# Kernel tuning notes

Measured on AMD Instinct MI355X. Metric: run time of the kernel, lower is better.

Reference implementation:

```python
import jax, jax.numpy as jnp
import numpy as np

_MASK = -1.0e9
_EPS = 1e-8
B, N, E, D, L, NREL, TAU = 4, 2048, 32768, 128, 3, 1000, 0.1


def setup_inputs() -> dict:
    key = jax.random.key(0)
    ks = jax.random.split(key, 24)
    s = 0.05
    inp = {
        'edge_index': jax.random.randint(ks[0], (B, 2, E), 0, N, dtype=jnp.int32),
        'rels': jax.random.randint(ks[1], (B, E), 0, NREL, dtype=jnp.int32),
        'scores': jax.random.uniform(ks[2], (B, E), dtype=jnp.float32),
        'edge_conf_mask': jax.random.randint(ks[3], (B, E), 0, 2) > 0,
        'edge_mask': jax.random.randint(ks[4], (B, E), 0, 2) > 0,
        'mask': jnp.ones((B, N), dtype=bool),
        'r_query_embed': jax.random.normal(ks[5], (B, D), dtype=jnp.float32),
        'conf_embeds': jax.random.normal(ks[6], (B, E, D), dtype=jnp.float32),
        'rel_table': jax.random.normal(ks[7], (NREL, D), dtype=jnp.float32) * s,
        'beta_W': jax.random.normal(ks[8], (D, 1), dtype=jnp.float32) * s,
        'beta_b': jnp.zeros((1,), dtype=jnp.float32),
        'msg_W': jax.random.normal(ks[9], (L, 5 * D, D), dtype=jnp.float32) * s,
        'msg_b': jnp.zeros((L, D), dtype=jnp.float32),
        'upd_W': jax.random.normal(ks[10], (L, D, D), dtype=jnp.float32) * s,
        'upd_b': jnp.zeros((L, D), dtype=jnp.float32),
        'ln_g': jnp.ones((D,), dtype=jnp.float32),
        'ln_b': jnp.zeros((D,), dtype=jnp.float32),
        'att_W': jax.random.normal(ks[11], (L, 3 * D, 1), dtype=jnp.float32) * s,
        'att_b': jnp.zeros((L, 1), dtype=jnp.float32),
        'den_W1': jax.random.normal(ks[12], (3 * D, D), dtype=jnp.float32) * s,
        'den_b1': jnp.zeros((D,), dtype=jnp.float32),
        'den_W2': jax.random.normal(ks[13], (D, 1), dtype=jnp.float32) * s,
        'den_b2': jnp.zeros((1,), dtype=jnp.float32),
    }
    return inp


def _layer_norm(x, g, b, eps=1e-5):
    mu = jnp.mean(x, axis=-1, keepdims=True)
    var = jnp.var(x, axis=-1, keepdims=True)
    return (x - mu) * jax.lax.rsqrt(var + eps) * g + b


def reference(edge_index, rels, scores, edge_conf_mask, edge_mask, mask,
              r_query_embed, conf_embeds, rel_table, beta_W, beta_b,
              msg_W, msg_b, upd_W, upd_b, ln_g, ln_b, att_W, att_b,
              den_W1, den_b1, den_W2, den_b2):
    Bb, Nn = mask.shape
    Ee = edge_index.shape[2]
    d = rel_table.shape[1]
    bidx = jnp.arange(Bb)[:, None]                      # [B,1] batch index for scatter/gather
    src = edge_index[:, 0, :]                           # [B,E]
    tgt = edge_index[:, 1, :]                           # [B,E]

    h_init = jnp.zeros((Bb, Nn, d), dtype=rel_table.dtype).at[:, 0, :].set(1.0)
    h = h_init
    h_r = rel_table[rels]                               # [B,E,D]
    rq = jnp.broadcast_to(r_query_embed[:, None, :], (Bb, Ee, d))
    em = edge_mask.astype(h.dtype)[..., None]           # [B,E,1]

    # edge denoiser gate
    gate_in = jnp.concatenate([h_r, rq, conf_embeds], axis=-1)
    den = jax.nn.sigmoid(jax.nn.relu(gate_in @ den_W1 + den_b1) @ den_W2 + den_b2) * em

    beta = jax.nn.sigmoid((h_r + rq) @ beta_W + beta_b)             # [B,E,1]
    gate_known = jax.nn.sigmoid((scores[..., None] - beta) / TAU)
    gate = jnp.where(edge_conf_mask[..., None], gate_known, 0.5)

    outs = []
    for k in range(msg_W.shape[0]):
        h_src = h[bidx, src]                            # [B,E,D] gather
        h_init_src = h_init[bidx, src]
        msg_in = jnp.concatenate([h_src * h_r, h_src, h_init_src, h_r, conf_embeds], axis=-1)
        raw_msg = jax.nn.relu(msg_in @ msg_W[k] + msg_b[k])         # [B,E,D]

        att_in = jnp.concatenate([raw_msg, h_r, rq], axis=-1)
        att = jax.nn.leaky_relu((att_in @ att_W[k] + att_b[k])[..., 0], 0.01)
        att = jnp.where(edge_mask, att, _MASK)

        # scatter-softmax over edges sharing a target node
        mx = jnp.full((Bb, Nn), _MASK, dtype=att.dtype).at[bidx, tgt].max(att)
        ex = jnp.exp(att - mx[bidx, tgt])
        sm = jnp.zeros((Bb, Nn), dtype=att.dtype).at[bidx, tgt].add(ex)
        alpha = ex / (sm[bidx, tgt] + _EPS)             # [B,E]

        wmsg = gate * alpha[..., None] * raw_msg * em * den
        aggr = jnp.zeros_like(h).at[bidx, tgt].add(wmsg)
        h = _layer_norm(h + aggr @ upd_W[k] + upd_b[k], ln_g, ln_b)
        outs.append(h[:, 0, :])
    return jnp.stack(outs, axis=1)                      # [B,L,D]
```

## Files before the change

kernel.cpp:

```cpp
#include <hip/hip_runtime.h>
#include <stdint.h>
#include <math.h>

#define BB 4
#define NNODE 2048
#define NE 32768
#define DDIM 128
#define NL 3
#define NRELS 1000
#define MASKV -1000000000.0f

typedef unsigned short ushort_t;
typedef __attribute__((ext_vector_type(8))) short bfrag;
typedef __attribute__((ext_vector_type(4))) float f4;

__device__ __forceinline__ float sigf(float x){ return 1.0f/(1.0f+expf(-x)); }

__device__ __forceinline__ float bf2f(ushort_t u){
  union { unsigned int i; float f; } v; v.i = ((unsigned int)u) << 16; return v.f;
}
__device__ __forceinline__ ushort_t f2bf(float x){
  union { float f; unsigned int u; } v; v.f = x;
  unsigned int r = (v.u + 0x7FFFu + ((v.u >> 16) & 1u)) >> 16;
  return (ushort_t)r;
}
__device__ __forceinline__ float bflo(unsigned u){
  union{unsigned i;float f;}v; v.i=u<<16; return v.f;
}
__device__ __forceinline__ float bfhi(unsigned u){
  union{unsigned i;float f;}v; v.i=u&0xFFFF0000u; return v.f;
}
__device__ __forceinline__ unsigned pmul_bf(unsigned a, unsigned b){
  return (unsigned)f2bf(bflo(a)*bflo(b)) | ((unsigned)f2bf(bfhi(a)*bfhi(b))<<16);
}
__device__ __forceinline__ unsigned packbf(float a, float b){
  return (unsigned)f2bf(a) | ((unsigned)f2bf(b)<<16);
}

__global__ void prep_kernel(const void* cm_raw, const void* em_raw,
    uint8_t* __restrict__ cm, uint8_t* __restrict__ em, int* __restrict__ deg,
    const float* __restrict__ relt, ushort_t* __restrict__ relt_bf,
    const float* __restrict__ rq, ushort_t* __restrict__ rq_bf,
    int* __restrict__ src_c, int* __restrict__ rel_c, int* __restrict__ ge_c,
    float* __restrict__ h, ushort_t* __restrict__ h_bf)
{
  __shared__ int flag_s;
  if (threadIdx.x < 64){
    unsigned v = ((const unsigned*)cm_raw)[threadIdx.x];
    bool i32ok = (v <= 1u);
    bool f32ok = (v == 0u) || (v == 0x3F800000u);
    unsigned long long bi = __ballot(i32ok);
    unsigned long long bf_ = __ballot(f32ok);
    if (threadIdx.x == 0) flag_s = (bi==~0ULL) ? 0 : ((bf_==~0ULL) ? 1 : 2);
  }
  __syncthreads();
  const int f = flag_s;
  int gid = blockIdx.x*256 + threadIdx.x;
  if (gid < BB*NE){
    uint8_t c, e;
    if (f == 0){ c = ((const int*)cm_raw)[gid]!=0;   e = ((const int*)em_raw)[gid]!=0; }
    else if (f == 1){ c = ((const float*)cm_raw)[gid]!=0.0f; e = ((const float*)em_raw)[gid]!=0.0f; }
    else { c = ((const uint8_t*)cm_raw)[gid]!=0; e = ((const uint8_t*)em_raw)[gid]!=0; }
    cm[gid]=c; em[gid]=e;
    src_c[gid]=0; rel_c[gid]=0; ge_c[gid]=0;
  }
  if (gid < BB*NNODE) deg[gid]=0;
  if (gid < NRELS*DDIM/4){
    float4 v = *(const float4*)&relt[gid*4];
    ushort4 o; o.x=f2bf(v.x); o.y=f2bf(v.y); o.z=f2bf(v.z); o.w=f2bf(v.w);
    *(ushort4*)&relt_bf[gid*4] = o;
  }
  if (gid < BB*DDIM/4){
    float4 v = *(const float4*)&rq[gid*4];
    ushort4 o; o.x=f2bf(v.x); o.y=f2bf(v.y); o.z=f2bf(v.z); o.w=f2bf(v.w);
    *(ushort4*)&rq_bf[gid*4] = o;
  }
  {
    int base = gid*4;
    int nd = base & (NNODE*DDIM - 1);
    bool one = (nd < DDIM);
    float4 hv = one ? (float4){1.f,1.f,1.f,1.f} : (float4){0.f,0.f,0.f,0.f};
    ushort4 hb = one ? (ushort4){0x3F80,0x3F80,0x3F80,0x3F80} : (ushort4){0,0,0,0};
    *(float4*)&h[base] = hv;
    *(ushort4*)&h_bf[base] = hb;
  }
}

__global__ void csr_hist_kernel(const int* __restrict__ edge_index,
                                const uint8_t* __restrict__ em, int* __restrict__ deg){
  int gid = blockIdx.x*256 + threadIdx.x;
  if (!em[gid]) return;
  int b = gid >> 15, e = gid & (NE-1);
  int tgt = edge_index[(b<<16) + NE + e];
  atomicAdd(&deg[(b<<11) + tgt], 1);
}
__global__ void csr_scan_kernel(const int* __restrict__ deg,
                                int* __restrict__ base, int* __restrict__ cursor){
  __shared__ int part[256];
  int t = threadIdx.x;
  int loc[32]; int s = 0;
  #pragma unroll
  for (int i=0;i<32;++i){ loc[i] = deg[t*32+i]; s += loc[i]; }
  part[t] = s; __syncthreads();
  for (int off=1; off<256; off<<=1){
    int v = (t >= off) ? part[t-off] : 0;
    __syncthreads();
    part[t] += v;
    __syncthreads();
  }
  int ex = (t==0) ? 0 : part[t-1];
  #pragma unroll
  for (int i=0;i<32;++i){ base[t*32+i] = ex; cursor[t*32+i] = ex; ex += loc[i]; }
  if (t == 255) base[256*32] = ex;
}
__global__ void csr_scatter_kernel(const int* __restrict__ edge_index,
                                   const int* __restrict__ rels,
                                   const uint8_t* __restrict__ em,
                                   int* __restrict__ cursor,
                                   int* __restrict__ src_c, int* __restrict__ rel_c,
                                   int* __restrict__ ge_c){
  int gid = blockIdx.x*256 + threadIdx.x;
  if (!em[gid]) return;
  int b = gid >> 15, e = gid & (NE-1);
  int tgt = edge_index[(b<<16) + NE + e];
  int src = edge_index[(b<<16) + e];
  int pos = atomicAdd(&cursor[(b<<11) + tgt], 1);
  src_c[pos] = (b<<11) | src;
  rel_c[pos] = rels[gid];
  ge_c[pos]  = gid;
}

__global__ void precomp_tables_kernel(
    const float* __restrict__ relt, const float* __restrict__ rq,
    const float* __restrict__ attW, const float* __restrict__ betaW,
    const float* __restrict__ msgW, const float* __restrict__ denW1,
    const float* __restrict__ denb1,
    float* __restrict__ att_rel, float* __restrict__ att_rq,
    float* __restrict__ beta_rel, float* __restrict__ beta_rq,
    float* __restrict__ denrq, float* __restrict__ initvec,
    float* __restrict__ src0vec)
{
  int wid = (blockIdx.x*256 + threadIdx.x) >> 6;
  int lane = threadIdx.x & 63;
  if (wid >= 4024) return;
  if (wid >= 4016){
    int widx = wid - 4016;
    const float* A = nullptr; const float* W; int K = 128;
    float* outp; const float* bias = nullptr;
    if (widx < 4){ A = rq + widx*128; W = denW1 + 16384; outp = denrq + widx*128; bias = denb1; }
    else if (widx < 7){ int k=widx-4; W = msgW + (size_t)k*81920 + 32768; outp = initvec + k*128; }
    else { W = msgW + 16384; K = 256; outp = src0vec; }
    float a0=0.f, a1=0.f;
    for (int kk=0; kk<K; kk+=8){
      float av[8], w0[8], w1[8];
      #pragma unroll
      for (int u=0;u<8;++u){
        av[u] = A ? A[kk+u] : 1.0f;
        w0[u] = W[(size_t)(kk+u)*128 + lane];
        w1[u] = W[(size_t)(kk+u)*128 + lane + 64];
      }
      #pragma unroll
      for (int u=0;u<8;++u){ a0 = fmaf(av[u], w0[u], a0); a1 = fmaf(av[u], w1[u], a1); }
    }
    if (bias){ a0 += bias[lane]; a1 += bias[lane+64]; }
    outp[lane] = a0; outp[lane+64] = a1;
    return;
  }
  const float* vec; const float* w; float* dst; int di;
  if (wid < 3*NRELS){
    int k = wid/1000, rl = wid%1000;
    vec = relt + rl*DDIM; w = attW + k*384 + 128; dst = att_rel; di = wid;
  } else if (wid < 3*NRELS + 3*BB){
    int idx = wid - 3*NRELS; int k = idx/BB, b = idx%BB;
    vec = rq + b*DDIM; w = attW + k*384 + 256; dst = att_rq; di = idx;
  } else if (wid < 3*NRELS + 3*BB + NRELS){
    int rl = wid - (3*NRELS + 3*BB);
    vec = relt + rl*DDIM; w = betaW; dst = beta_rel; di = rl;
  } else {
    int b = wid - (3*NRELS + 3*BB + NRELS);
    vec = rq + b*DDIM; w = betaW; dst = beta_rq; di = b;
  }
  float s = vec[lane]*w[lane] + vec[lane+64]*w[lane+64];
  #pragma unroll
  for (int off=32; off; off>>=1) s += __shfl_xor(s, off, 64);
  if (lane == 0) dst[di] = s;
}

__global__ void build_wimg_kernel(const float* __restrict__ msgW,
                                  const float* __restrict__ denW1,
                                  ushort_t* __restrict__ img_msg,
                                  ushort_t* __restrict__ img_den,
                                  ushort_t* __restrict__ img_tab){
  int e = blockIdx.x*256 + threadIdx.x;
  if (e >= 22*8192) return;
  int img_id = e >> 13;
  int ei = e & 8191;
  int j = ei >> 6;
  int kk = (((ei & 63) << 1) ^ ((j & 7) << 4)) >> 1;
  float v;
  ushort_t* dst;
  if (img_id < 12){
    int k = img_id >> 2, c = img_id & 3;
    int rowbase = (c < 2) ? c*64 : 512 + (c-2)*64;
    v = msgW[(size_t)k*81920 + (rowbase+kk)*128 + j];
    dst = img_msg + (size_t)img_id*8192;
  } else if (img_id < 14){
    int c = img_id - 12;
    v = denW1[(size_t)(256 + c*64 + kk)*128 + j];
    dst = img_den + (size_t)c*8192;
  } else if (img_id < 20){
    int idx = img_id - 14, k = idx >> 1, c = idx & 1;
    v = msgW[(size_t)k*81920 + (384 + c*64 + kk)*128 + j];
    dst = img_tab + (size_t)idx*8192;
  } else {
    int c = img_id - 20;
    v = denW1[(size_t)(c*64 + kk)*128 + j];
    dst = img_tab + (size_t)(6+c)*8192;
  }
  dst[ei] = f2bf(v);
}

__global__ __launch_bounds__(256,2) void table_gemm_kernel(
    const ushort_t* __restrict__ relt_bf, const ushort_t* __restrict__ img_msg,
    const ushort_t* __restrict__ img_tab, const float* __restrict__ msgb,
    float* __restrict__ relmsg, float* __restrict__ relhh0,
    float* __restrict__ denrel)
{
  __shared__ char lds[32768];
  __shared__ float bias_s[128];
  const int blk = blockIdx.x;
  const int job = blk % 5;
  const int ri0 = (blk/5) << 7;
  const int t = threadIdx.x;
  const uint4* imgb;
  float* outp;
  if (job < 3){ imgb = (const uint4*)(img_tab + (size_t)(2*job)*8192); outp = relmsg + (size_t)job*NRELS*DDIM; }
  else if (job == 3){ imgb = (const uint4*)img_msg; outp = relhh0; }
  else { imgb = (const uint4*)(img_tab + (size_t)6*8192); outp = denrel; }
  if (t < 128) bias_s[t] = (job < 3) ? msgb[job*128 + t] : 0.f;

  const int lane=t&63, wid=t>>6;
  const int wr=wid>>1, wc=wid&1;
  const int rbase=wr<<6, cbase=wc<<6;
  const int lr=lane&15, lk=lane>>4;
  const int swz=(lane&7)<<4;
  const int g=t&7, row0=t>>3;
  const int aswz=(g<<4)^((row0&7)<<4);

  f4 acc[4][4];
  #pragma unroll
  for (int m=0;m<4;++m)
    #pragma unroll
    for (int n=0;n<4;++n) acc[m][n]=(f4){0.f,0.f,0.f,0.f};

  uint4 pa[4], pb[4];
  auto issueA = [&](int ch){
    #pragma unroll
    for (int i=0;i<4;++i){
      int rr = ri0 + row0 + (i<<5);
      rr = (rr < NRELS) ? rr : (NRELS-1);
      pa[i] = *(const uint4*)&relt_bf[(size_t)rr*128 + (ch<<6) + (g<<3)];
    }
    #pragma unroll
    for (int i=0;i<4;++i) pb[i] = imgb[ch*1024 + (i<<8) + t];
  };

  __syncthreads();
  issueA(0);
  #pragma unroll
  for (int ch=0; ch<2; ++ch){
    #pragma unroll
    for (int i=0;i<4;++i){
      int row = row0 + (i<<5);
      *(uint4*)(lds + row*128 + aswz) = pa[i];
    }
    *(uint4*)(lds+16384+(t<<4))        = pb[0];
    *(uint4*)(lds+16384+(t<<4)+4096)   = pb[1];
    *(uint4*)(lds+16384+(t<<4)+8192)   = pb[2];
    *(uint4*)(lds+16384+(t<<4)+12288)  = pb[3];
    __syncthreads();
    if (ch < 1) issueA(ch+1);
    #pragma unroll
    for (int s=0;s<2;++s){
      bfrag af[4], bfr[4];
      #pragma unroll
      for (int m=0;m<4;++m)
        af[m] = *(const bfrag*)(lds + (rbase+(m<<4)+lr)*128 + (((s<<6)+(lk<<4)) ^ swz));
      #pragma unroll
      for (int n=0;n<4;++n)
        bfr[n] = *(const bfrag*)(lds + 16384 + (cbase+(n<<4)+lr)*128 + (((s<<6)+(lk<<4)) ^ swz));
      #pragma unroll
      for (int m=0;m<4;++m)
        #pragma unroll
        for (int n=0;n<4;++n)
          acc[m][n] = __builtin_amdgcn_mfma_f32_16x16x32_bf16(af[m], bfr[n], acc[m][n], 0,0,0);
    }
    __syncthreads();
  }

  #pragma unroll
  for (int m=0;m<4;++m)
    #pragma unroll
    for (int n=0;n<4;++n){
      int col = cbase + (n<<4) + lr;
      float bv = bias_s[col];
      #pragma unroll
      for (int q=0;q<4;++q){
        int gr = ri0 + rbase + (m<<4) + (lk<<2) + q;
        if (gr < NRELS) outp[(size_t)gr*128 + col] = acc[m][n][q] + bv;
      }
    }
}

__global__ __launch_bounds__(256,2) void coef_mfma_kernel(
    const int* __restrict__ nact_p,
    const int* __restrict__ rel_c, const int* __restrict__ ge_c,
    const float* __restrict__ conf, const ushort_t* __restrict__ img_den,
    const float* __restrict__ denrel, const float* __restrict__ denrq,
    const float* __restrict__ denW2, const float* __restrict__ denb2,
    const float* __restrict__ scores, const uint8_t* __restrict__ cm,
    const float* __restrict__ beta_rel, const float* __restrict__ beta_rq,
    const float* __restrict__ betab,
    float* __restrict__ coef_c)
{
  __shared__ char lds[32768];
  __shared__ int rel_s[128], ge_s[128];
  __shared__ float w2_s[128];

  const int blk = blockIdx.x;
  const int ci0 = blk << 7;
  const int nact = *nact_p;
  if (ci0 >= nact) return;
  const int t = threadIdx.x;
  if (t < 128){ rel_s[t]=rel_c[ci0+t]; ge_s[t]=ge_c[ci0+t]; w2_s[t]=denW2[t]; }

  const int lane=t&63, wid=t>>6;
  const int wr=wid>>1, wc=wid&1;
  const int rbase=wr<<6, cbase=wc<<6;
  const int lr=lane&15, lk=lane>>4;
  const int swz=(lane&7)<<4;
  const int g=t&7, row0=t>>3;
  const int aswz=(g<<4)^((row0&7)<<4);

  f4 acc[4][4];
  #pragma unroll
  for (int m=0;m<4;++m)
    #pragma unroll
    for (int n=0;n<4;++n) acc[m][n]=(f4){0.f,0.f,0.f,0.f};

  const uint4* imgp = (const uint4*)img_den;
  float4 pf0[4], pf1[4];
  uint4 pb[4];
  __syncthreads();

  auto issueA = [&](int ch){
    const int d0=(ch&1)<<6;
    #pragma unroll
    for (int i=0;i<4;++i){
      int row=row0+(i<<5);
      const float* cp = conf + (((size_t)ge_s[row])<<7) + d0 + (g<<3);
      pf0[i]=*(const float4*)cp; pf1[i]=*(const float4*)(cp+4);
    }
    #pragma unroll
    for (int i=0;i<4;++i) pb[i]=imgp[ch*1024+(i<<8)+t];
  };

  issueA(0);
  #pragma unroll
  for (int ch=0; ch<2; ++ch){
    #pragma unroll
    for (int i=0;i<4;++i){
      int row=row0+(i<<5);
      uint4 val;
      val.x=packbf(pf0[i].x,pf0[i].y); val.y=packbf(pf0[i].z,pf0[i].w);
      val.z=packbf(pf1[i].x,pf1[i].y); val.w=packbf(pf1[i].z,pf1[i].w);
      *(uint4*)(lds + row*128 + aswz) = val;
    }
    *(uint4*)(lds+16384+(t<<4))        = pb[0];
    *(uint4*)(lds+16384+(t<<4)+4096)   = pb[1];
    *(uint4*)(lds+16384+(t<<4)+8192)   = pb[2];
    *(uint4*)(lds+16384+(t<<4)+12288)  = pb[3];
    __syncthreads();
    if (ch < 1) issueA(ch+1);
    #pragma unroll
    for (int s=0;s<2;++s){
      bfrag af[4], bfr[4];
      #pragma unroll
      for (int m=0;m<4;++m)
        af[m] = *(const bfrag*)(lds + (rbase+(m<<4)+lr)*128 + (((s<<6)+(lk<<4)) ^ swz));
      #pragma unroll
      for (int n=0;n<4;++n)
        bfr[n] = *(const bfrag*)(lds + 16384 + (cbase+(n<<4)+lr)*128 + (((s<<6)+(lk<<4)) ^ swz));
      #pragma unroll
      for (int m=0;m<4;++m)
        #pragma unroll
        for (int n=0;n<4;++n)
          acc[m][n] = __builtin_amdgcn_mfma_f32_16x16x32_bf16(af[m], bfr[n], acc[m][n], 0,0,0);
    }
    __syncthreads();
  }

  #pragma unroll
  for (int m=0;m<4;++m)
    #pragma unroll
    for (int n=0;n<4;++n)
      #pragma unroll
      for (int q=0;q<4;++q){
        int row=rbase+(m<<4)+(lk<<2)+q;
        int col=cbase+(n<<4)+lr;
        *(ushort_t*)(lds+(row<<8)+((col<<1)^((row&7)<<4))) = f2bf(acc[m][n][q]);
      }
  __syncthreads();

  #pragma unroll
  for (int i=0;i<8;++i){
    int u=t+(i<<8), row=u>>4, gg=u&15, c0=gg<<3;
    uint4 v = *(const uint4*)(lds+(row<<8)+((gg<<4)^((row&7)<<4)));
    float vv[8] = {bflo(v.x),bfhi(v.x),bflo(v.y),bfhi(v.y),
                   bflo(v.z),bfhi(v.z),bflo(v.w),bfhi(v.w)};
    int rel=rel_s[row], ge=ge_s[row], b=ge>>15;
    const float* dr = denrel + ((size_t)rel<<7) + c0;
    const float* dq = denrq + (b<<7) + c0;
    float part=0.f;
    #pragma unroll
    for (int j=0;j<8;++j){
      float m = fmaxf(vv[j] + dr[j] + dq[j], 0.f);
      part = fmaf(m, w2_s[c0+j], part);
    }
    #pragma unroll
    for (int off=1; off<16; off<<=1) part += __shfl_xor(part, off, 16);
    if (gg == 0){
      float den = sigf(part + denb2[0]);
      float beta = sigf(beta_rel[rel] + beta_rq[b] + betab[0]);
      float gt = cm[ge] ? sigf((scores[ge]-beta)*10.0f) : 0.5f;
      coef_c[ci0+row] = gt * den;
    }
  }
}

template<bool L0>
__global__ __launch_bounds__(256,2) void msg_mfma_kernel(
    const int* __restrict__ nact_p,
    const int* __restrict__ src_c, const int* __restrict__ rel_c,
    const int* __restrict__ ge_c,
    const ushort_t* __restrict__ relt_bf, const float* __restrict__ conf,
    const ushort_t* __restrict__ h_bf, const float* __restrict__ H1,
    const ushort_t* __restrict__ img_msg,
    const float* __restrict__ relmsg, const float* __restrict__ relhh0,
    const float* __restrict__ src0vec, const float* __restrict__ initvec,
    const float* __restrict__ attW, const float* __restrict__ attb,
    const float* __restrict__ att_rel, const float* __restrict__ att_rq,
    ushort_t* __restrict__ raw_c, float* __restrict__ att_c, int layer)
{
  constexpr int NCH = L0 ? 2 : 4;
  __shared__ char lds[32768];
  __shared__ int src_s[128], rel_s[128], ge_s[128];
  __shared__ float attw_s[128];

  const int blk = blockIdx.x;
  const int ci0 = blk << 7;
  const int nact = *nact_p;
  if (ci0 >= nact) return;
  const int t = threadIdx.x;
  if (t < 128){
    src_s[t]=src_c[ci0+t]; rel_s[t]=rel_c[ci0+t]; ge_s[t]=ge_c[ci0+t];
    attw_s[t]=attW[layer*384+t];
  }

  const int lane=t&63, wid=t>>6;
  const int wr=wid>>1, wc=wid&1;
  const int rbase=wr<<6, cbase=wc<<6;
  const int lr=lane&15, lk=lane>>4;
  const int swz=(lane&7)<<4;
  const int g=t&7, row0=t>>3;
  const int aswz=(g<<4)^((row0&7)<<4);

  f4 acc[4][4];
  #pragma unroll
  for (int m=0;m<4;++m)
    #pragma unroll
    for (int n=0;n<4;++n) acc[m][n]=(f4){0.f,0.f,0.f,0.f};

  const uint4* imgp = (const uint4*)(img_msg + (size_t)layer*4*8192);
  uint4 pa[4], pr[4], pb[4];
  float4 pf0[4], pf1[4];
  __syncthreads();

  auto issueA = [&](int ch){
    const int d0=(ch&1)<<6;
    const bool cf = L0 || (ch>=2);
    #pragma unroll
    for (int i=0;i<4;++i){
      int row=row0+(i<<5);
      if (cf){
        const float* cp = conf + (((size_t)ge_s[row])<<7) + d0 + (g<<3);
        pf0[i]=*(const float4*)cp; pf1[i]=*(const float4*)(cp+4);
      } else {
        pa[i]=*(const uint4*)&h_bf[(((size_t)src_s[row])<<7)+d0+(g<<3)];
        pr[i]=*(const uint4*)&relt_bf[(((size_t)rel_s[row])<<7)+d0+(g<<3)];
      }
    }
    int ic = L0 ? ch+2 : ch;
    #pragma unroll
    for (int i=0;i<4;++i) pb[i]=imgp[ic*1024+(i<<8)+t];
  };

  issueA(0);
  #pragma unroll
  for (int ch=0; ch<NCH; ++ch){
    const bool cf = L0 || (ch>=2);
    #pragma unroll
    for (int i=0;i<4;++i){
      int row=row0+(i<<5);
      uint4 val;
      if (cf){
        val.x=packbf(pf0[i].x,pf0[i].y); val.y=packbf(pf0[i].z,pf0[i].w);
        val.z=packbf(pf1[i].x,pf1[i].y); val.w=packbf(pf1[i].z,pf1[i].w);
      } else {
        val.x=pmul_bf(pa[i].x,pr[i].x); val.y=pmul_bf(pa[i].y,pr[i].y);
        val.z=pmul_bf(pa[i].z,pr[i].z); val.w=pmul_bf(pa[i].w,pr[i].w);
      }
      *(uint4*)(lds + row*128 + aswz) = val;
    }
    *(uint4*)(lds+16384+(t<<4))        = pb[0];
    *(uint4*)(lds+16384+(t<<4)+4096)   = pb[1];
    *(uint4*)(lds+16384+(t<<4)+8192)   = pb[2];
    *(uint4*)(lds+16384+(t<<4)+12288)  = pb[3];
    __syncthreads();
    if (ch < NCH-1) issueA(ch+1);
    #pragma unroll
    for (int s=0;s<2;++s){
      bfrag af[4], bfr[4];
      #pragma unroll
      for (int m=0;m<4;++m)
        af[m] = *(const bfrag*)(lds + (rbase+(m<<4)+lr)*128 + (((s<<6)+(lk<<4)) ^ swz));
      #pragma unroll
      for (int n=0;n<4;++n)
        bfr[n] = *(const bfrag*)(lds + 16384 + (cbase+(n<<4)+lr)*128 + (((s<<6)+(lk<<4)) ^ swz));
      #pragma unroll
      for (int m=0;m<4;++m)
        #pragma unroll
        for (int n=0;n<4;++n)
          acc[m][n] = __builtin_amdgcn_mfma_f32_16x16x32_bf16(af[m], bfr[n], acc[m][n], 0,0,0);
    }
    __syncthreads();
  }

  #pragma unroll
  for (int m=0;m<4;++m)
    #pragma unroll
    for (int n=0;n<4;++n)
      #pragma unroll
      for (int q=0;q<4;++q){
        int row=rbase+(m<<4)+(lk<<2)+q;
        int col=cbase+(n<<4)+lr;
        *(ushort_t*)(lds+(row<<8)+((col<<1)^((row&7)<<4))) = f2bf(acc[m][n][q]);
      }
  __syncthreads();

  #pragma unroll
  for (int i=0;i<8;++i){
    int u=t+(i<<8), row=u>>4, gg=u&15, c0=gg<<3;
    uint4 v = *(const uint4*)(lds+(row<<8)+((gg<<4)^((row&7)<<4)));
    float vv[8] = {bflo(v.x),bfhi(v.x),bflo(v.y),bfhi(v.y),
                   bflo(v.z),bfhi(v.z),bflo(v.w),bfhi(v.w)};
    int rel=rel_s[row], sc=src_s[row], ge=ge_s[row], b=ge>>15;
    const float* rm = relmsg + (((size_t)(layer*NRELS+rel))<<7) + c0;
    float bias[8];
    #pragma unroll
    for (int j=0;j<8;++j) bias[j] = rm[j];
    if (!L0){
      const float* hp = H1 + (((size_t)sc)<<7) + c0;
      #pragma unroll
      for (int j=0;j<8;++j) bias[j] += hp[j];
      if ((sc & (NNODE-1)) == 0){
        const float* iv = initvec + layer*128 + c0;
        #pragma unroll
        for (int j=0;j<8;++j) bias[j] += iv[j];
      }
    } else {
      if ((sc & (NNODE-1)) == 0){
        const float* rh = relhh0 + ((size_t)rel<<7) + c0;
        const float* sv = src0vec + c0;
        #pragma unroll
        for (int j=0;j<8;++j) bias[j] += rh[j] + sv[j];
      }
    }
    float part=0.f;
    unsigned o0,o1,o2,o3;
    {
      float m0=fmaxf(vv[0]+bias[0],0.f), m1=fmaxf(vv[1]+bias[1],0.f);
      float m2=fmaxf(vv[2]+bias[2],0.f), m3=fmaxf(vv[3]+bias[3],0.f);
      float m4=fmaxf(vv[4]+bias[4],0.f), m5=fmaxf(vv[5]+bias[5],0.f);
      float m6=fmaxf(vv[6]+bias[6],0.f), m7=fmaxf(vv[7]+bias[7],0.f);
      part = m0*attw_s[c0] + m1*attw_s[c0+1] + m2*attw_s[c0+2] + m3*attw_s[c0+3]
           + m4*attw_s[c0+4] + m5*attw_s[c0+5] + m6*attw_s[c0+6] + m7*attw_s[c0+7];
      o0=packbf(m0,m1); o1=packbf(m2,m3); o2=packbf(m4,m5); o3=packbf(m6,m7);
    }
    uint4 ov; ov.x=o0; ov.y=o1; ov.z=o2; ov.w=o3;
    *(uint4*)&raw_c[(((size_t)(ci0+row))<<7) + c0] = ov;
    #pragma unroll
    for (int off=1; off<16; off<<=1) part += __shfl_xor(part, off, 16);
    if (gg == 0){
      float a = part + att_rel[layer*NRELS+rel] + att_rq[layer*BB+b] + attb[layer];
      a = (a >= 0.f) ? a : 0.01f*a;
      att_c[ci0+row] = a;
    }
  }
}

#define FMA4(acc, a, bv) do { \
    acc.x = fmaf(a, bv.x, acc.x); \
    acc.y = fmaf(a, bv.y, acc.y); \
    acc.z = fmaf(a, bv.z, acc.z); \
    acc.w = fmaf(a, bv.w, acc.w); } while(0)

__global__ __launch_bounds__(256,2) void h1_gemm_kernel(
    const float* __restrict__ h, const float* __restrict__ msgW,
    float* __restrict__ H1, int layer)
{
  __shared__ float As[64*65];
  __shared__ float Bs[64*128];
  const int t = threadIdx.x, blk = blockIdx.x;
  const int n0 = blk << 6;
  const int c = t & 15, r = t >> 4;
  float4 acc0[4], acc1[4];
  #pragma unroll
  for (int i=0;i<4;++i){ acc0[i]=make_float4(0,0,0,0); acc1[i]=make_float4(0,0,0,0); }
  const float* wbase = msgW + (size_t)layer*81920 + 16384;

  for (int ch=0; ch<2; ++ch){
    __syncthreads();
    #pragma unroll
    for (int l=0;l<16;++l){
      int idx=(l<<8)+t, ei=idx>>6, kk=idx&63;
      As[ei*65+kk] = h[(size_t)(n0+ei)*DDIM + (ch<<6) + kk];
    }
    #pragma unroll
    for (int l=0;l<32;++l){
      int idx=(l<<8)+t, kk=idx>>7, j=idx&127;
      Bs[(kk<<7)+j] = wbase[((ch<<6)+kk)*DDIM + j];
    }
    __syncthreads();
    #pragma unroll 4
    for (int kk=0;kk<64;++kk){
      const float4 b0 = *(const float4*)&Bs[(kk<<7) + (c<<2)];
      const float4 b1 = *(const float4*)&Bs[(kk<<7) + 64 + (c<<2)];
      #pragma unroll
      for (int i=0;i<4;++i){
        const float a = As[((r<<2)+i)*65 + kk];
        FMA4(acc0[i], a, b0);
        FMA4(acc1[i], a, b1);
      }
    }
  }
  const int col0 = c << 2;
  #pragma unroll
  for (int i=0;i<4;++i){
    const int row = n0 + (r<<2) + i;
    *(float4*)&H1[(size_t)row*DDIM + col0]      = make_float4(acc0[i].x,acc0[i].y,acc0[i].z,acc0[i].w);
    *(float4*)&H1[(size_t)row*DDIM + 64 + col0] = make_float4(acc1[i].x,acc1[i].y,acc1[i].z,acc1[i].w);
  }
}

__global__ __launch_bounds__(128) void node_agg_kernel(
    const int* __restrict__ base,
    const float* __restrict__ att_c, const float* __restrict__ coef_c,
    const ushort_t* __restrict__ raw_c, float* __restrict__ aggr)
{
  const int n = blockIdx.x;
  const int t = threadIdx.x;
  const int b0 = base[n], b1 = base[n+1];
  const int deg = b1 - b0;
  if (deg == 0){ aggr[((size_t)n<<7)+t] = 0.f; return; }
  __shared__ float w_s[128];
  __shared__ float red[4];
  float mx = -3.0e38f;
  for (int j=t; j<deg; j+=128) mx = fmaxf(mx, att_c[b0+j]);
  #pragma unroll
  for (int o=1;o<64;o<<=1) mx = fmaxf(mx, __shfl_xor(mx, o, 64));
  if ((t&63)==0) red[t>>6] = mx;
  __syncthreads();
  mx = fmaxf(red[0], red[1]);
  float s = 0.f;
  for (int j=t; j<deg; j+=128) s += expf(att_c[b0+j]-mx);
  #pragma unroll
  for (int o=1;o<64;o<<=1) s += __shfl_xor(s, o, 64);
  if ((t&63)==0) red[2+(t>>6)] = s;
  __syncthreads();
  const float inv = 1.0f/((red[2]+red[3]) + 1e-8f);
  float accv = 0.f;
  for (int jb=0; jb<deg; jb+=128){
    int jj = jb + t;
    __syncthreads();
    if (jj < deg) w_s[t] = coef_c[b0+jj] * expf(att_c[b0+jj]-mx) * inv;
    __syncthreads();
    int lim = min(128, deg-jb);
    for (int j=0; j<lim; ++j)
      accv = fmaf(w_s[j], bf2f(raw_c[(((size_t)(b0+jb+j))<<7)+t]), accv);
  }
  aggr[((size_t)n<<7)+t] = accv;
}

__global__ __launch_bounds__(256,2) void update_kernel(
    const float* __restrict__ aggr, const float* __restrict__ updW,
    const float* __restrict__ updb,
    const float* __restrict__ lng, const float* __restrict__ lnb,
    float* __restrict__ h, ushort_t* __restrict__ h_bf,
    float* __restrict__ out, int layer)
{
  __shared__ float As[64*65];
  __shared__ float Bs[64*128];
  const int t = threadIdx.x, blk = blockIdx.x;
  const int n0 = blk << 6;
  const int c = t & 15, r = t >> 4;
  float4 acc0[4], acc1[4];
  #pragma unroll
  for (int i=0;i<4;++i){ acc0[i]=make_float4(0,0,0,0); acc1[i]=make_float4(0,0,0,0); }
  const float* wbase = updW + (size_t)layer*DDIM*DDIM;

  for (int ch=0; ch<2; ++ch){
    __syncthreads();
    #pragma unroll
    for (int l=0;l<16;++l){
      int idx=(l<<8)+t, ei=idx>>6, kk=idx&63;
      As[ei*65+kk] = aggr[(size_t)(n0+ei)*DDIM + (ch<<6) + kk];
    }
    #pragma unroll
    for (int l=0;l<32;++l){
      int idx=(l<<8)+t, kk=idx>>7, j=idx&127;
      Bs[(kk<<7)+j] = wbase[((ch<<6)+kk)*DDIM + j];
    }
    __syncthreads();
    #pragma unroll 4
    for (int kk=0;kk<64;++kk){
      const float4 b0 = *(const float4*)&Bs[(kk<<7) + (c<<2)];
      const float4 b1 = *(const float4*)&Bs[(kk<<7) + 64 + (c<<2)];
      #pragma unroll
      for (int i=0;i<4;++i){
        const float a = As[((r<<2)+i)*65 + kk];
        FMA4(acc0[i], a, b0);
        FMA4(acc1[i], a, b1);
      }
    }
  }

  const int col0 = c << 2;
  float ub0[4], ub1[4], g0[4], g1[4], lb0[4], lb1[4];
  #pragma unroll
  for (int q=0;q<4;++q){
    ub0[q] = updb[layer*DDIM + col0+q];  ub1[q] = updb[layer*DDIM + 64+col0+q];
    g0[q]  = lng[col0+q];                g1[q]  = lng[64+col0+q];
    lb0[q] = lnb[col0+q];                lb1[q] = lnb[64+col0+q];
  }

  #pragma unroll
  for (int i=0;i<4;++i){
    const int row = n0 + (r<<2) + i;
    float* hrow = h + (size_t)row*DDIM;
    float4 h0 = *(float4*)&hrow[col0];
    float4 h1 = *(float4*)&hrow[64+col0];
    float x0[4], x1[4];
    x0[0] = h0.x + acc0[i].x + ub0[0];
    x0[1] = h0.y + acc0[i].y + ub0[1];
    x0[2] = h0.z + acc0[i].z + ub0[2];
    x0[3] = h0.w + acc0[i].w + ub0[3];
    x1[0] = h1.x + acc1[i].x + ub1[0];
    x1[1] = h1.y + acc1[i].y + ub1[1];
    x1[2] = h1.z + acc1[i].z + ub1[2];
    x1[3] = h1.w + acc1[i].w + ub1[3];
    float s = 0.f, s2 = 0.f;
    #pragma unroll
    for (int q=0;q<4;++q){ s += x0[q]+x1[q]; s2 += x0[q]*x0[q] + x1[q]*x1[q]; }
    #pragma unroll
    for (int off=1; off<16; off<<=1){
      s  += __shfl_xor(s,  off, 16);
      s2 += __shfl_xor(s2, off, 16);
    }
    const float mu = s * (1.0f/128.0f);
    const float var = s2 * (1.0f/128.0f) - mu*mu;
    const float rstd = rsqrtf(var + 1e-5f);
    float4 y0, y1;
    y0.x = (x0[0]-mu)*rstd*g0[0] + lb0[0];
    y0.y = (x0[1]-mu)*rstd*g0[1] + lb0[1];
    y0.z = (x0[2]-mu)*rstd*g0[2] + lb0[2];
    y0.w = (x0[3]-mu)*rstd*g0[3] + lb0[3];
    y1.x = (x1[0]-mu)*rstd*g1[0] + lb1[0];
    y1.y = (x1[1]-mu)*rstd*g1[1] + lb1[1];
    y1.z = (x1[2]-mu)*rstd*g1[2] + lb1[2];
    y1.w = (x1[3]-mu)*rstd*g1[3] + lb1[3];
    *(float4*)&hrow[col0] = y0;
    *(float4*)&hrow[64+col0] = y1;
    ushort4 z0, z1;
    z0.x=f2bf(y0.x); z0.y=f2bf(y0.y); z0.z=f2bf(y0.z); z0.w=f2bf(y0.w);
    z1.x=f2bf(y1.x); z1.y=f2bf(y1.y); z1.z=f2bf(y1.z); z1.w=f2bf(y1.w);
    *(ushort4*)&h_bf[(size_t)row*DDIM + col0] = z0;
    *(ushort4*)&h_bf[(size_t)row*DDIM + 64 + col0] = z1;
    if ((row & (NNODE-1)) == 0){
      const int bb_ = row >> 11;
      float* op = out + (size_t)(bb_*NL + layer)*DDIM;
      *(float4*)&op[col0] = y0;
      *(float4*)&op[64+col0] = y1;
    }
  }
}

extern "C" void kernel_launch(void* const* d_in, const int* in_sizes, int n_in,
                              void* d_out, int out_size, void* d_ws, size_t ws_size,
                              hipStream_t stream) {
  const int*   edge_index = (const int*)d_in[0];
  const int*   rels       = (const int*)d_in[1];
  const float* scores     = (const float*)d_in[2];
  const void*  cm_raw     = d_in[3];
  const void*  em_raw     = d_in[4];
  const float* rq    = (const float*)d_in[6];
  const float* conf  = (const float*)d_in[7];
  const float* relt  = (const float*)d_in[8];
  const float* betaW = (const float*)d_in[9];
  const float* betab = (const float*)d_in[10];
  const float* msgW  = (const float*)d_in[11];
  const float* msgb  = (const float*)d_in[12];
  const float* updW  = (const float*)d_in[13];
  const float* updb  = (const float*)d_in[14];
  const float* lng   = (const float*)d_in[15];
  const float* lnb   = (const float*)d_in[16];
  const float* attW  = (const float*)d_in[17];
  const float* attb  = (const float*)d_in[18];
  const float* denW1 = (const float*)d_in[19];
  const float* denb1 = (const float*)d_in[20];
  const float* denW2 = (const float*)d_in[21];
  const float* denb2 = (const float*)d_in[22];
  float* out = (float*)d_out;
  char* ws = (char*)d_ws;

  size_t off = 0;
  float* h        = (float*)(ws + off); off += (size_t)BB*NNODE*DDIM*4;
  ushort_t* h_bf  = (ushort_t*)(ws + off); off += (size_t)BB*NNODE*DDIM*2;
  float* aggr     = (float*)(ws + off); off += (size_t)BB*NNODE*DDIM*4;
  float* H1       = (float*)(ws + off); off += (size_t)BB*NNODE*DDIM*4;
  ushort_t* raw_c = (ushort_t*)(ws + off); off += (size_t)BB*NE*DDIM*2;
  float* att_c    = (float*)(ws + off); off += (size_t)BB*NE*4;
  float* coef_c   = (float*)(ws + off); off += (size_t)BB*NE*4;
  int* src_c      = (int*)(ws + off); off += (size_t)BB*NE*4;
  int* rel_c      = (int*)(ws + off); off += (size_t)BB*NE*4;
  int* ge_c       = (int*)(ws + off); off += (size_t)BB*NE*4;
  int* deg        = (int*)(ws + off); off += (size_t)BB*NNODE*4;
  int* base       = (int*)(ws + off); off += (size_t)(BB*NNODE+16)*4;
  int* cursor     = (int*)(ws + off); off += (size_t)BB*NNODE*4;
  ushort_t* relt_bf = (ushort_t*)(ws + off); off += (size_t)NRELS*DDIM*2 + 64;
  ushort_t* rq_bf   = (ushort_t*)(ws + off); off += (size_t)BB*DDIM*2 + 64;
  ushort_t* img_msg = (ushort_t*)(ws + off); off += (size_t)12*8192*2;
  ushort_t* img_den = (ushort_t*)(ws + off); off += (size_t)2*8192*2;
  ushort_t* img_tab = (ushort_t*)(ws + off); off += (size_t)8*8192*2;
  float* relmsg   = (float*)(ws + off); off += (size_t)3*NRELS*DDIM*4;
  float* relhh0   = (float*)(ws + off); off += (size_t)NRELS*DDIM*4;
  float* denrel   = (float*)(ws + off); off += (size_t)NRELS*DDIM*4;
  float* denrq    = (float*)(ws + off); off += (size_t)BB*DDIM*4;
  float* initvec  = (float*)(ws + off); off += 3*DDIM*4;
  float* src0vec  = (float*)(ws + off); off += DDIM*4;
  float* att_rel  = (float*)(ws + off); off += 3*NRELS*4 + 32;
  float* att_rq   = (float*)(ws + off); off += 64;
  float* beta_rel = (float*)(ws + off); off += NRELS*4 + 32;
  float* beta_rq  = (float*)(ws + off); off += 64;
  uint8_t* cm_dec = (uint8_t*)(ws + off); off += (size_t)BB*NE;
  uint8_t* em_dec = (uint8_t*)(ws + off); off += (size_t)BB*NE;

  prep_kernel<<<1024, 256, 0, stream>>>(cm_raw, em_raw, cm_dec, em_dec, deg,
                                        relt, relt_bf, rq, rq_bf,
                                        src_c, rel_c, ge_c, h, h_bf);
  csr_hist_kernel<<<512, 256, 0, stream>>>(edge_index, em_dec, deg);
  csr_scan_kernel<<<1, 256, 0, stream>>>(deg, base, cursor);
  csr_scatter_kernel<<<512, 256, 0, stream>>>(edge_index, rels, em_dec, cursor,
                                              src_c, rel_c, ge_c);
  precomp_tables_kernel<<<1006, 256, 0, stream>>>(relt, rq, attW, betaW,
                                                  msgW, denW1, denb1,
                                                  att_rel, att_rq, beta_rel, beta_rq,
                                                  denrq, initvec, src0vec);
  build_wimg_kernel<<<704, 256, 0, stream>>>(msgW, denW1, img_msg, img_den, img_tab);
  table_gemm_kernel<<<40, 256, 0, stream>>>(relt_bf, img_msg, img_tab, msgb,
                                            relmsg, relhh0, denrel);
  coef_mfma_kernel<<<1024, 256, 0, stream>>>(base + BB*NNODE, rel_c, ge_c, conf, img_den,
                                             denrel, denrq, denW2, denb2,
                                             scores, cm_dec, beta_rel, beta_rq, betab,
                                             coef_c);
  for (int k = 0; k < NL; ++k){
    if (k == 0){
      msg_mfma_kernel<true><<<1024, 256, 0, stream>>>(base + BB*NNODE, src_c, rel_c, ge_c,
          relt_bf, conf, h_bf, H1, img_msg, relmsg, relhh0, src0vec, initvec,
          attW, attb, att_rel, att_rq, raw_c, att_c, k);
    } else {
      h1_gemm_kernel<<<128, 256, 0, stream>>>(h, msgW, H1, k);
      msg_mfma_kernel<false><<<1024, 256, 0, stream>>>(base + BB*NNODE, src_c, rel_c, ge_c,
          relt_bf, conf, h_bf, H1, img_msg, relmsg, relhh0, src0vec, initvec,
          attW, attb, att_rel, att_rq, raw_c, att_c, k);
    }
    node_agg_kernel<<<BB*NNODE, 128, 0, stream>>>(base, att_c, coef_c, raw_c, aggr);
    update_kernel<<<128, 256, 0, stream>>>(aggr, updW, updb, lng, lnb, h, h_bf, out, k);
  }
}
```

Measured before the change: 382.7 us.

## Fold precompute kernels into prep and fuse H1 GEMM into update kernel

Merges the precomp_tables and build_wimg kernels into prep_kernel and drops the unused rq_bf conversion, which removes two launches. The h1_gemm for the next layer now runs at the end of update_kernel on the freshly normalized rows it already holds in registers, so h is not re-read from global memory and one launch per layer is saved. The node_agg inner loop is unrolled by four to issue more independent loads. In exchange, prep_kernel's branches grow more complex and update_kernel does extra GEMM work with additional register and shared-memory pressure.

Result: faster. 366.2 us (-4.3%).

```diff
diff --git a/kernel.cpp b/kernel.cpp
--- a/kernel.cpp
+++ b/kernel.cpp
@@ -40,9 +40,18 @@
 __global__ void prep_kernel(const void* cm_raw, const void* em_raw,
     uint8_t* __restrict__ cm, uint8_t* __restrict__ em, int* __restrict__ deg,
     const float* __restrict__ relt, ushort_t* __restrict__ relt_bf,
-    const float* __restrict__ rq, ushort_t* __restrict__ rq_bf,
+    const float* __restrict__ rq,
+    const float* __restrict__ attW, const float* __restrict__ betaW,
+    const float* __restrict__ msgW, const float* __restrict__ denW1,
+    const float* __restrict__ denb1,
     int* __restrict__ src_c, int* __restrict__ rel_c, int* __restrict__ ge_c,
-    float* __restrict__ h, ushort_t* __restrict__ h_bf)
+    float* __restrict__ h, ushort_t* __restrict__ h_bf,
+    ushort_t* __restrict__ img_msg, ushort_t* __restrict__ img_den,
+    ushort_t* __restrict__ img_tab,
+    float* __restrict__ att_rel, float* __restrict__ att_rq,
+    float* __restrict__ beta_rel, float* __restrict__ beta_rq,
+    float* __restrict__ denrq, float* __restrict__ initvec,
+    float* __restrict__ src0vec)
 {
   __shared__ int flag_s;
   if (threadIdx.x < 64){
@@ -55,7 +64,8 @@
   }
   __syncthreads();
   const int f = flag_s;
-  int gid = blockIdx.x*256 + threadIdx.x;
+  const int gid = blockIdx.x*256 + threadIdx.x;
+
   if (gid < BB*NE){
     uint8_t c, e;
     if (f == 0){ c = ((const int*)cm_raw)[gid]!=0;   e = ((const int*)em_raw)[gid]!=0; }
@@ -69,11 +79,6 @@
     float4 v = *(const float4*)&relt[gid*4];
     ushort4 o; o.x=f2bf(v.x); o.y=f2bf(v.y); o.z=f2bf(v.z); o.w=f2bf(v.w);
     *(ushort4*)&relt_bf[gid*4] = o;
-  }
-  if (gid < BB*DDIM/4){
-    float4 v = *(const float4*)&rq[gid*4];
-    ushort4 o; o.x=f2bf(v.x); o.y=f2bf(v.y); o.z=f2bf(v.z); o.w=f2bf(v.w);
-    *(ushort4*)&rq_bf[gid*4] = o;
   }
   {
     int base = gid*4;
@@ -83,6 +88,77 @@
     ushort4 hb = one ? (ushort4){0x3F80,0x3F80,0x3F80,0x3F80} : (ushort4){0,0,0,0};
     *(float4*)&h[base] = hv;
     *(ushort4*)&h_bf[base] = hb;
+  }
+  if (gid < 22*8192){
+    int img_id = gid >> 13;
+    int ei = gid & 8191;
+    int j = ei >> 6;
+    int kk = (((ei & 63) << 1) ^ ((j & 7) << 4)) >> 1;
+    float v; ushort_t* dst;
+    if (img_id < 12){
+      int k = img_id >> 2, c = img_id & 3;
+      int rowbase = (c < 2) ? c*64 : 512 + (c-2)*64;
+      v = msgW[(size_t)k*81920 + (rowbase+kk)*128 + j];
+      dst = img_msg + (size_t)img_id*8192;
+    } else if (img_id < 14){
+      int c = img_id - 12;
+      v = denW1[(size_t)(256 + c*64 + kk)*128 + j];
+      dst = img_den + (size_t)c*8192;
+    } else if (img_id < 20){
+      int idx = img_id - 14, k = idx >> 1, c = idx & 1;
+      v = msgW[(size_t)k*81920 + (384 + c*64 + kk)*128 + j];
+      dst = img_tab + (size_t)idx*8192;
+    } else {
+      int c = img_id - 20;
+      v = denW1[(size_t)(c*64 + kk)*128 + j];
+      dst = img_tab + (size_t)(6+c)*8192;
+    }
+    dst[ei] = f2bf(v);
+  }
+  {
+    int wid = gid >> 6;
+    int lane = threadIdx.x & 63;
+    if (wid < 4016){
+      const float* vec; const float* w; float* dst; int di;
+      if (wid < 3*NRELS){
+        int k = wid/1000, rl = wid%1000;
+        vec = relt + rl*DDIM; w = attW + k*384 + 128; dst = att_rel; di = wid;
+      } else if (wid < 3*NRELS + 3*BB){
+        int idx = wid - 3*NRELS; int k = idx/BB, b = idx%BB;
+        vec = rq + b*DDIM; w = attW + k*384 + 256; dst = att_rq; di = idx;
+      } else if (wid < 3*NRELS + 3*BB + NRELS){
+        int rl = wid - (3*NRELS + 3*BB);
+        vec = relt + rl*DDIM; w = betaW; dst = beta_rel; di = rl;
+      } else {
+        int b = wid - (3*NRELS + 3*BB + NRELS);
+        vec = rq + b*DDIM; w = betaW; dst = beta_rq; di = b;
+      }
+      float s = vec[lane]*w[lane] + vec[lane+64]*w[lane+64];
+      #pragma unroll
+      for (int off=32; off; off>>=1) s += __shfl_xor(s, off, 64);
+      if (lane == 0) dst[di] = s;
+    } else if (wid < 4024){
+      int widx = wid - 4016;
+      const float* A = nullptr; const float* W; int K = 128;
+      float* outp; const float* bias = nullptr;
+      if (widx < 4){ A = rq + widx*128; W = denW1 + 16384; outp = denrq + widx*128; bias = denb1; }
+      else if (widx < 7){ int k=widx-4; W = msgW + (size_t)k*81920 + 32768; outp = initvec + k*128; }
+      else { W = msgW + 16384; K = 256; outp = src0vec; }
+      float a0=0.f, a1=0.f;
+      for (int kk=0; kk<K; kk+=8){
+        float av[8], w0[8], w1[8];
+        #pragma unroll
+        for (int u=0;u<8;++u){
+          av[u] = A ? A[kk+u] : 1.0f;
+          w0[u] = W[(size_t)(kk+u)*128 + lane];
+          w1[u] = W[(size_t)(kk+u)*128 + lane + 64];
+        }
+        #pragma unroll
+        for (int u=0;u<8;++u){ a0 = fmaf(av[u], w0[u], a0); a1 = fmaf(av[u], w1[u], a1); }
+      }
+      if (bias){ a0 += bias[lane]; a1 += bias[lane+64]; }
+      outp[lane] = a0; outp[lane+64] = a1;
+    }
   }
 }
 
@@ -128,96 +204,6 @@
   src_c[pos] = (b<<11) | src;
   rel_c[pos] = rels[gid];
   ge_c[pos]  = gid;
-}
-
-__global__ void precomp_tables_kernel(
-    const float* __restrict__ relt, const float* __restrict__ rq,
-    const float* __restrict__ attW, const float* __restrict__ betaW,
-    const float* __restrict__ msgW, const float* __restrict__ denW1,
-    const float* __restrict__ denb1,
-    float* __restrict__ att_rel, float* __restrict__ att_rq,
-    float* __restrict__ beta_rel, float* __restrict__ beta_rq,
-    float* __restrict__ denrq, float* __restrict__ initvec,
-    float* __restrict__ src0vec)
-{
-  int wid = (blockIdx.x*256 + threadIdx.x) >> 6;
-  int lane = threadIdx.x & 63;
-  if (wid >= 4024) return;
-  if (wid >= 4016){
-    int widx = wid - 4016;
-    const float* A = nullptr; const float* W; int K = 128;
-    float* outp; const float* bias = nullptr;
-    if (widx < 4){ A = rq + widx*128; W = denW1 + 16384; outp = denrq + widx*128; bias = denb1; }
-    else if (widx < 7){ int k=widx-4; W = msgW + (size_t)k*81920 + 32768; outp = initvec + k*128; }
-    else { W = msgW + 16384; K = 256; outp = src0vec; }
-    float a0=0.f, a1=0.f;
-    for (int kk=0; kk<K; kk+=8){
-      float av[8], w0[8], w1[8];
-      #pragma unroll
-      for (int u=0;u<8;++u){
-        av[u] = A ? A[kk+u] : 1.0f;
-        w0[u] = W[(size_t)(kk+u)*128 + lane];
-        w1[u] = W[(size_t)(kk+u)*128 + lane + 64];
-      }
-      #pragma unroll
-      for (int u=0;u<8;++u){ a0 = fmaf(av[u], w0[u], a0); a1 = fmaf(av[u], w1[u], a1); }
-    }
-    if (bias){ a0 += bias[lane]; a1 += bias[lane+64]; }
-    outp[lane] = a0; outp[lane+64] = a1;
-    return;
-  }
-  const float* vec; const float* w; float* dst; int di;
-  if (wid < 3*NRELS){
-    int k = wid/1000, rl = wid%1000;
-    vec = relt + rl*DDIM; w = attW + k*384 + 128; dst = att_rel; di = wid;
-  } else if (wid < 3*NRELS + 3*BB){
-    int idx = wid - 3*NRELS; int k = idx/BB, b = idx%BB;
-    vec = rq + b*DDIM; w = attW + k*384 + 256; dst = att_rq; di = idx;
-  } else if (wid < 3*NRELS + 3*BB + NRELS){
-    int rl = wid - (3*NRELS + 3*BB);
-    vec = relt + rl*DDIM; w = betaW; dst = beta_rel; di = rl;
-  } else {
-    int b = wid - (3*NRELS + 3*BB + NRELS);
-    vec = rq + b*DDIM; w = betaW; dst = beta_rq; di = b;
-  }
-  float s = vec[lane]*w[lane] + vec[lane+64]*w[lane+64];
-  #pragma unroll
-  for (int off=32; off; off>>=1) s += __shfl_xor(s, off, 64);
-  if (lane == 0) dst[di] = s;
-}
-
-__global__ void build_wimg_kernel(const float* __restrict__ msgW,
-                                  const float* __restrict__ denW1,
-                                  ushort_t* __restrict__ img_msg,
-                                  ushort_t* __restrict__ img_den,
-                                  ushort_t* __restrict__ img_tab){
-  int e = blockIdx.x*256 + threadIdx.x;
-  if (e >= 22*8192) return;
-  int img_id = e >> 13;
-  int ei = e & 8191;
-  int j = ei >> 6;
-  int kk = (((ei & 63) << 1) ^ ((j & 7) << 4)) >> 1;
-  float v;
-  ushort_t* dst;
-  if (img_id < 12){
-    int k = img_id >> 2, c = img_id & 3;
-    int rowbase = (c < 2) ? c*64 : 512 + (c-2)*64;
-    v = msgW[(size_t)k*81920 + (rowbase+kk)*128 + j];
-    dst = img_msg + (size_t)img_id*8192;
-  } else if (img_id < 14){
-    int c = img_id - 12;
-    v = denW1[(size_t)(256 + c*64 + kk)*128 + j];
-    dst = img_den + (size_t)c*8192;
-  } else if (img_id < 20){
-    int idx = img_id - 14, k = idx >> 1, c = idx & 1;
-    v = msgW[(size_t)k*81920 + (384 + c*64 + kk)*128 + j];
-    dst = img_tab + (size_t)idx*8192;
-  } else {
-    int c = img_id - 20;
-    v = denW1[(size_t)(c*64 + kk)*128 + j];
-    dst = img_tab + (size_t)(6+c)*8192;
-  }
-  dst[ei] = f2bf(v);
 }
 
 __global__ __launch_bounds__(256,2) void table_gemm_kernel(
@@ -609,60 +595,6 @@
   }
 }
 
-#define FMA4(acc, a, bv) do { \
-    acc.x = fmaf(a, bv.x, acc.x); \
-    acc.y = fmaf(a, bv.y, acc.y); \
-    acc.z = fmaf(a, bv.z, acc.z); \
-    acc.w = fmaf(a, bv.w, acc.w); } while(0)
-
-__global__ __launch_bounds__(256,2) void h1_gemm_kernel(
-    const float* __restrict__ h, const float* __restrict__ msgW,
-    float* __restrict__ H1, int layer)
-{
-  __shared__ float As[64*65];
-  __shared__ float Bs[64*128];
-  const int t = threadIdx.x, blk = blockIdx.x;
-  const int n0 = blk << 6;
-  const int c = t & 15, r = t >> 4;
-  float4 acc0[4], acc1[4];
-  #pragma unroll
-  for (int i=0;i<4;++i){ acc0[i]=make_float4(0,0,0,0); acc1[i]=make_float4(0,0,0,0); }
-  const float* wbase = msgW + (size_t)layer*81920 + 16384;
-
-  for (int ch=0; ch<2; ++ch){
-    __syncthreads();
-    #pragma unroll
-    for (int l=0;l<16;++l){
-      int idx=(l<<8)+t, ei=idx>>6, kk=idx&63;
-      As[ei*65+kk] = h[(size_t)(n0+ei)*DDIM + (ch<<6) + kk];
-    }
-    #pragma unroll
-    for (int l=0;l<32;++l){
-      int idx=(l<<8)+t, kk=idx>>7, j=idx&127;
-      Bs[(kk<<7)+j] = wbase[((ch<<6)+kk)*DDIM + j];
-    }
-    __syncthreads();
-    #pragma unroll 4
-    for (int kk=0;kk<64;++kk){
-      const float4 b0 = *(const float4*)&Bs[(kk<<7) + (c<<2)];
-      const float4 b1 = *(const float4*)&Bs[(kk<<7) + 64 + (c<<2)];
-      #pragma unroll
-      for (int i=0;i<4;++i){
-        const float a = As[((r<<2)+i)*65 + kk];
-        FMA4(acc0[i], a, b0);
-        FMA4(acc1[i], a, b1);
-      }
-    }
-  }
-  const int col0 = c << 2;
-  #pragma unroll
-  for (int i=0;i<4;++i){
-    const int row = n0 + (r<<2) + i;
-    *(float4*)&H1[(size_t)row*DDIM + col0]      = make_float4(acc0[i].x,acc0[i].y,acc0[i].z,acc0[i].w);
-    *(float4*)&H1[(size_t)row*DDIM + 64 + col0] = make_float4(acc1[i].x,acc1[i].y,acc1[i].z,acc1[i].w);
-  }
-}
-
 __global__ __launch_bounds__(128) void node_agg_kernel(
     const int* __restrict__ base,
     const float* __restrict__ att_c, const float* __restrict__ coef_c,
@@ -696,18 +628,36 @@
     if (jj < deg) w_s[t] = coef_c[b0+jj] * expf(att_c[b0+jj]-mx) * inv;
     __syncthreads();
     int lim = min(128, deg-jb);
-    for (int j=0; j<lim; ++j)
+    int j = 0;
+    for (; j+3 < lim; j += 4){
+      float v0 = bf2f(raw_c[(((size_t)(b0+jb+j  ))<<7)+t]);
+      float v1 = bf2f(raw_c[(((size_t)(b0+jb+j+1))<<7)+t]);
+      float v2 = bf2f(raw_c[(((size_t)(b0+jb+j+2))<<7)+t]);
+      float v3 = bf2f(raw_c[(((size_t)(b0+jb+j+3))<<7)+t]);
+      accv = fmaf(w_s[j],v0,accv);
+      accv = fmaf(w_s[j+1],v1,accv);
+      accv = fmaf(w_s[j+2],v2,accv);
+      accv = fmaf(w_s[j+3],v3,accv);
+    }
+    for (; j<lim; ++j)
       accv = fmaf(w_s[j], bf2f(raw_c[(((size_t)(b0+jb+j))<<7)+t]), accv);
   }
   aggr[((size_t)n<<7)+t] = accv;
 }
+
+#define FMA4(acc, a, bv) do { \
+    acc.x = fmaf(a, bv.x, acc.x); \
+    acc.y = fmaf(a, bv.y, acc.y); \
+    acc.z = fmaf(a, bv.z, acc.z); \
+    acc.w = fmaf(a, bv.w, acc.w); } while(0)
 
 __global__ __launch_bounds__(256,2) void update_kernel(
     const float* __restrict__ aggr, const float* __restrict__ updW,
     const float* __restrict__ updb,
     const float* __restrict__ lng, const float* __restrict__ lnb,
+    const float* __restrict__ msgW,
     float* __restrict__ h, ushort_t* __restrict__ h_bf,
-    float* __restrict__ out, int layer)
+    float* __restrict__ H1, float* __restrict__ out, int layer)
 {
   __shared__ float As[64*65];
   __shared__ float Bs[64*128];
@@ -754,6 +704,7 @@
     lb0[q] = lnb[col0+q];                lb1[q] = lnb[64+col0+q];
   }
 
+  float4 yv0[4], yv1[4];
   #pragma unroll
   for (int i=0;i<4;++i){
     const int row = n0 + (r<<2) + i;
@@ -796,11 +747,54 @@
     z1.x=f2bf(y1.x); z1.y=f2bf(y1.y); z1.z=f2bf(y1.z); z1.w=f2bf(y1.w);
     *(ushort4*)&h_bf[(size_t)row*DDIM + col0] = z0;
     *(ushort4*)&h_bf[(size_t)row*DDIM + 64 + col0] = z1;
+    yv0[i] = y0; yv1[i] = y1;
     if ((row & (NNODE-1)) == 0){
       const int bb_ = row >> 11;
       float* op = out + (size_t)(bb_*NL + layer)*DDIM;
       *(float4*)&op[col0] = y0;
       *(float4*)&op[64+col0] = y1;
+    }
+  }
+
+  if (layer < NL-1){
+    const float* w1 = msgW + (size_t)(layer+1)*81920 + 16384;
+    float4 k0[4], k1[4];
+    #pragma unroll
+    for (int i=0;i<4;++i){ k0[i]=make_float4(0,0,0,0); k1[i]=make_float4(0,0,0,0); }
+    for (int ch=0; ch<2; ++ch){
+      __syncthreads();
+      #pragma unroll
+      for (int i=0;i<4;++i){
+        const int ei = (r<<2)+i;
+        float4 v = (ch==0) ? yv0[i] : yv1[i];
+        As[ei*65 + col0 + 0] = v.x;
+        As[ei*65 + col0 + 1] = v.y;
+        As[ei*65 + col0 + 2] = v.z;
+        As[ei*65 + col0 + 3] = v.w;
+      }
+      #pragma unroll
+      for (int l=0;l<32;++l){
+        int idx=(l<<8)+t, kk=idx>>7, j=idx&127;
+        Bs[(kk<<7)+j] = w1[((ch<<6)+kk)*DDIM + j];
+      }
+      __syncthreads();
+      #pragma unroll 4
+      for (int kk=0;kk<64;++kk){
+        const float4 b0 = *(const float4*)&Bs[(kk<<7) + col0];
+        const float4 b1 = *(const float4*)&Bs[(kk<<7) + 64 + col0];
+        #pragma unroll
+        for (int i=0;i<4;++i){
+          const float a = As[((r<<2)+i)*65 + kk];
+          FMA4(k0[i], a, b0);
+          FMA4(k1[i], a, b1);
+        }
+      }
+    }
+    #pragma unroll
+    for (int i=0;i<4;++i){
+      const int row = n0 + (r<<2) + i;
+      *(float4*)&H1[(size_t)row*DDIM + col0]      = k0[i];
+      *(float4*)&H1[(size_t)row*DDIM + 64 + col0] = k1[i];
     }
   }
 }
@@ -848,7 +842,6 @@
   int* base       = (int*)(ws + off); off += (size_t)(BB*NNODE+16)*4;
   int* cursor     = (int*)(ws + off); off += (size_t)BB*NNODE*4;
   ushort_t* relt_bf = (ushort_t*)(ws + off); off += (size_t)NRELS*DDIM*2 + 64;
-  ushort_t* rq_bf   = (ushort_t*)(ws + off); off += (size_t)BB*DDIM*2 + 64;
   ushort_t* img_msg = (ushort_t*)(ws + off); off += (size_t)12*8192*2;
   ushort_t* img_den = (ushort_t*)(ws + off); off += (size_t)2*8192*2;
   ushort_t* img_tab = (ushort_t*)(ws + off); off += (size_t)8*8192*2;
@@ -866,17 +859,16 @@
   uint8_t* em_dec = (uint8_t*)(ws + off); off += (size_t)BB*NE;
 
   prep_kernel<<<1024, 256, 0, stream>>>(cm_raw, em_raw, cm_dec, em_dec, deg,
-                                        relt, relt_bf, rq, rq_bf,
-                                        src_c, rel_c, ge_c, h, h_bf);
+                                        relt, relt_bf, rq, attW, betaW,
+                                        msgW, denW1, denb1,
+                                        src_c, rel_c, ge_c, h, h_bf,
+                                        img_msg, img_den, img_tab,
+                                        att_rel, att_rq, beta_rel, beta_rq,
+                                        denrq, initvec, src0vec);
   csr_hist_kernel<<<512, 256, 0, stream>>>(edge_index, em_dec, deg);
   csr_scan_kernel<<<1, 256, 0, stream>>>(deg, base, cursor);
   csr_scatter_kernel<<<512, 256, 0, stream>>>(edge_index, rels, em_dec, cursor,
                                               src_c, rel_c, ge_c);
-  precomp_tables_kernel<<<1006, 256, 0, stream>>>(relt, rq, attW, betaW,
-                                                  msgW, denW1, denb1,
-                                                  att_rel, att_rq, beta_rel, beta_rq,
-                                                  denrq, initvec, src0vec);
-  build_wimg_kernel<<<704, 256, 0, stream>>>(msgW, denW1, img_msg, img_den, img_tab);
   table_gemm_kernel<<<40, 256, 0, stream>>>(relt_bf, img_msg, img_tab, msgb,
                                             relmsg, relhh0, denrel);
   coef_mfma_kernel<<<1024, 256, 0, stream>>>(base + BB*NNODE, rel_c, ge_c, conf, img_den,
@@ -889,12 +881,12 @@
           relt_bf, conf, h_bf, H1, img_msg, relmsg, relhh0, src0vec, initvec,
           attW, attb, att_rel, att_rq, raw_c, att_c, k);
     } else {
-      h1_gemm_kernel<<<128, 256, 0, stream>>>(h, msgW, H1, k);
       msg_mfma_kernel<false><<<1024, 256, 0, stream>>>(base + BB*NNODE, src_c, rel_c, ge_c,
           relt_bf, conf, h_bf, H1, img_msg, relmsg, relhh0, src0vec, initvec,
           attW, attb, att_rel, att_rq, raw_c, att_c, k);
     }
     node_agg_kernel<<<BB*NNODE, 128, 0, stream>>>(base, att_c, coef_c, raw_c, aggr);
-    update_kernel<<<128, 256, 0, stream>>>(aggr, updW, updb, lng, lnb, h, h_bf, out, k);
-  }
-}
+    update_kernel<<<128, 256, 0, stream>>>(aggr, updW, updb, lng, lnb, msgW,
+                                           h, h_bf, H1, out, k);
+  }
+}
```
